# Kernel tuning notes

Hardware: AMD Instinct MI355X
Metric: run time of the kernel (lower is better)

The kernel has to match this reference:

```python
import jax, jax.numpy as jnp
import numpy as np
from jax import lax

B, L, D, C = 4096, 50, 128, 64
V = 100000
H = D // 2  # bidirectional LSTM hidden size; 2*H == emb_dim


def setup_inputs() -> dict:
    key = jax.random.key(0)
    ks = jax.random.split(key, 26)
    f = lambda k, s: jax.random.normal(k, s, dtype=jnp.float32) * 0.05
    return {
        "r_idx": jax.random.randint(ks[0], (B,), 0, V),
        "a_idx": jax.random.randint(ks[1], (B,), 0, V),
        "acc_idx": jax.random.randint(ks[2], (B,), 0, V),
        "rank_q": jax.random.normal(ks[3], (B, L, D), dtype=jnp.float32),
        "rank_q_len": jax.random.randint(ks[4], (B,), 0, L),
        "ru_emb": f(ks[5], (V, D)),
        "au_emb": f(ks[6], (V, D)),
        "Wih_f": f(ks[7], (4 * H, D)), "Whh_f": f(ks[8], (4 * H, H)),
        "bih_f": f(ks[9], (4 * H,)), "bhh_f": f(ks[10], (4 * H,)),
        "Wih_b": f(ks[11], (4 * H, D)), "Whh_b": f(ks[12], (4 * H, H)),
        "bih_b": f(ks[13], (4 * H,)), "bhh_b": f(ks[14], (4 * H,)),
        "conv1_w": f(ks[15], (C, 1, D)), "conv1_b": f(ks[16], (C,)),
        "conv2_w": f(ks[17], (C, 2, D)), "conv2_b": f(ks[18], (C,)),
        "conv3_w": f(ks[19], (C, 3, D)), "conv3_b": f(ks[20], (C,)),
        "fc1_w": f(ks[21], (6,)), "fc1_b": f(ks[22], (1,)),
        "fc2_w": f(ks[23], (C,)), "fc2_b": f(ks[24], (1,)),
    }


def _lstm_dir(x, Wih, Whh, bih, bhh, reverse):
    # x: [B, L, D] -> outputs [B, L, H]; PyTorch gate order i,f,g,o
    b = x.shape[0]
    xs = jnp.swapaxes(x, 0, 1)  # [L, B, D]
    h0 = jnp.zeros((b, Whh.shape[1]), x.dtype)

    def step(carry, xt):
        h, c = carry
        gates = xt @ Wih.T + h @ Whh.T + (bih + bhh)
        i, fg, g, o = jnp.split(gates, 4, axis=-1)
        i = jax.nn.sigmoid(i)
        fg = jax.nn.sigmoid(fg)
        g = jnp.tanh(g)
        o = jax.nn.sigmoid(o)
        c = fg * c + i * g
        h = o * jnp.tanh(c)
        return (h, c), h

    _, ys = lax.scan(step, (h0, h0), xs, reverse=reverse)
    return jnp.swapaxes(ys, 0, 1)


def _score(mat, conv1_w, conv1_b, conv2_w, conv2_b, conv3_w, conv3_b, fc1_w, fc1_b, fc2_w, fc2_b):
    # mat: [B, 3, D]; three tiny conv branches (kernel heights 1/2/3, width=D)
    branches = []
    for w, bias in ((conv1_w, conv1_b), (conv2_w, conv2_b), (conv3_w, conv3_b)):
        k = w.shape[1]
        wins = jnp.stack([mat[:, i:i + k] for i in range(3 - k + 1)], axis=1)  # [B, W, k, D]
        branches.append(jax.nn.relu(jnp.einsum('bwkd,ckd->bcw', wins, w) + bias[None, :, None]))
    s = jnp.concatenate(branches, axis=2)  # [B, C, 6]
    h = jnp.einsum('bcw,w->bc', s, fc1_w) + fc1_b[0]  # fc_new_1: 6 -> 1
    return jnp.einsum('bc,c->b', h, fc2_w) + fc2_b[0]  # fc_new_2: C -> 1


def reference(r_idx, a_idx, acc_idx, rank_q, rank_q_len, ru_emb, au_emb,
              Wih_f, Whh_f, bih_f, bhh_f, Wih_b, Whh_b, bih_b, bhh_b,
              conv1_w, conv1_b, conv2_w, conv2_b, conv3_w, conv3_b,
              fc1_w, fc1_b, fc2_w, fc2_b):
    emb_r = ru_emb[r_idx]
    emb_a = au_emb[a_idx]
    emb_acc = au_emb[acc_idx]
    # bidirectional LSTM over the question sequence
    out_f = _lstm_dir(rank_q, Wih_f, Whh_f, bih_f, bhh_f, reverse=False)
    out_b = _lstm_dir(rank_q, Wih_b, Whh_b, bih_b, bhh_b, reverse=True)
    q_out = jnp.concatenate([out_f, out_b], axis=-1)  # [B, L, D]
    # prepend a zero timestep, then gather per-example at index rank_q_len
    q_pad = jnp.concatenate([jnp.zeros((q_out.shape[0], 1, q_out.shape[2]), q_out.dtype), q_out], axis=1)
    emb_q = q_pad[jnp.arange(q_pad.shape[0]), rank_q_len]  # [B, D]
    low = jnp.stack([emb_r, emb_q, emb_a], axis=1)   # [B, 3, D]
    high = jnp.stack([emb_r, emb_q, emb_acc], axis=1)
    fcp = (conv1_w, conv1_b, conv2_w, conv2_b, conv3_w, conv3_b, fc1_w, fc1_b, fc2_w, fc2_b)
    low_s = _score(low, *fcp)
    high_s = _score(high, *fcp)
    return jnp.sum(low_s - high_s)
```

## Files before the change

### kernel.cpp

```cpp
#include <hip/hip_runtime.h>
#include <hip/hip_bf16.h>

#define LSEQ 50
#define BATCH 4096

typedef __attribute__((ext_vector_type(8))) short bf16x8;
typedef __attribute__((ext_vector_type(4))) float f32x4;

__device__ __forceinline__ unsigned cvtpk(float lo, float hi) {
    unsigned r;
    asm("v_cvt_pk_bf16_f32 %0, %1, %2" : "=v"(r) : "v"(lo), "v"(hi));
    return r;
}
__device__ __forceinline__ bf16x8 pack8(float4 a, float4 b) {
    uint4 u;
    u.x = cvtpk(a.x, a.y); u.y = cvtpk(a.z, a.w);
    u.z = cvtpk(b.x, b.y); u.w = cvtpk(b.z, b.w);
    return __builtin_bit_cast(bf16x8, u);
}
__device__ __forceinline__ float fsigm(float x) {
    return __builtin_amdgcn_rcpf(1.0f + __builtin_amdgcn_exp2f(-1.44269504f * x));
}
__device__ __forceinline__ float ftanh(float x) {
    float e = __builtin_amdgcn_exp2f(2.88539008f * x);
    return 1.0f - 2.0f * __builtin_amdgcn_rcpf(e + 1.0f);
}

__global__ __launch_bounds__(256)
void sort_kernel(const int* __restrict__ qlen, int* __restrict__ perm)
{
    __shared__ int base[64];
    const int tid = threadIdx.x;
    if (tid < 64) base[tid] = 0;
    __syncthreads();
    for (int i = tid; i < BATCH; i += 256) atomicAdd(&base[qlen[i]], 1);
    __syncthreads();
    if (tid == 0) {
        int s = 0;
        for (int v = 0; v < 50; ++v) { int c = base[v]; base[v] = s; s += c; }
    }
    __syncthreads();
    for (int i = tid; i < BATCH; i += 256) {
        int pos = atomicAdd(&base[qlen[i]], 1);
        perm[pos] = i;
    }
}

__global__ __launch_bounds__(256, 2)
void lstm_kernel(const float* __restrict__ rank_q, const int* __restrict__ qlen,
                 const int* __restrict__ perm,
                 const float* __restrict__ Wih_f, const float* __restrict__ Whh_f,
                 const float* __restrict__ bih_f, const float* __restrict__ bhh_f,
                 const float* __restrict__ Wih_b, const float* __restrict__ Whh_b,
                 const float* __restrict__ bih_b, const float* __restrict__ bhh_b,
                 float* __restrict__ embq)
{
    const int grp = blockIdx.x;
    const int b0  = grp << 4;
    const int tid = threadIdx.x;
    const int wv  = tid >> 6;
    const int ln  = tid & 63;
    const int lm  = ln & 15;
    const int lq  = ln >> 4;
    const int m   = (wv << 4) + lm;

    __shared__ __align__(16) unsigned short xbuf[3][16][136];
    __shared__ __align__(16) unsigned short hbuf[2][16][72];
    __shared__ int len_s[16];

    if (tid < 16) len_s[tid] = qlen[perm[b0 + tid]];

    int exq[4], len_e[4];
    #pragma unroll
    for (int r = 0; r < 4; ++r) {
        exq[r]   = perm[b0 + (lq << 2) + r];
        len_e[r] = qlen[exq[r]];
    }

    const int se  = tid >> 4;
    const int exs = perm[b0 + se];
    const int sd  = (tid & 15) << 3;

    __syncthreads();

    int mx = 0, mn = 51;
    #pragma unroll
    for (int i = 0; i < 16; ++i) {
        const int l = len_s[i];
        mx = max(mx, l);
        mn = min(mn, l ? l : 51);
    }

    const int xoff = lm * 136 + (lq << 3);
    const int hoff = lm * 72 + (lq << 3);

    for (int dir = 0; dir < 2; ++dir) {
        const float* Wih = dir ? Wih_b : Wih_f;
        const float* Whh = dir ? Whh_b : Whh_f;
        const float* bih = dir ? bih_b : bih_f;
        const float* bhh = dir ? bhh_b : bhh_f;

        bf16x8 bfrag[4][6];
        float bias[4];
        #pragma unroll
        for (int j = 0; j < 4; ++j) {
            const int n = (j << 6) + m;
            bias[j] = bih[n] + bhh[n];
            #pragma unroll
            for (int s = 0; s < 6; ++s) {
                const int kb = (s << 5) + (lq << 3);
                const float* src = (s < 4) ? (Wih + n * 128 + kb)
                                           : (Whh + n * 64 + (kb - 128));
                bfrag[j][s] = pack8(*(const float4*)src, *(const float4*)(src + 4));
            }
        }

        const int steps = dir ? ((mn == 51) ? 0 : 51 - mn) : mx;

        float cst[4]  = {0.f, 0.f, 0.f, 0.f};
        float qval[4] = {0.f, 0.f, 0.f, 0.f};

        for (int i = tid; i < 16 * 72; i += 256) ((unsigned short*)hbuf)[i] = 0;

        const int tstep = dir ? -128 : 128;
        const float* gp = rank_q + ((size_t)exs * LSEQ + (dir ? LSEQ - 1 : 0)) * 128 + sd;

        float4 ha, hb2;
        if (steps > 0) {
            float4 a0 = *(const float4*)gp, b0v = *(const float4*)(gp + 4); gp += tstep;
            float4 a1 = *(const float4*)gp, b1v = *(const float4*)(gp + 4); gp += tstep;
            *(bf16x8*)&xbuf[0][se][sd] = pack8(a0, b0v);
            *(bf16x8*)&xbuf[1][se][sd] = pack8(a1, b1v);
            if (3 <= steps) { ha = *(const float4*)gp; hb2 = *(const float4*)(gp + 4); gp += tstep; }
        }
        __syncthreads();

        if (steps > 0) {
            f32x4 accx[4];
            {
                const unsigned short* xb = &xbuf[0][0][0];
                bf16x8 x0 = *(const bf16x8*)(xb + xoff);
                bf16x8 x1 = *(const bf16x8*)(xb + xoff + 32);
                bf16x8 x2 = *(const bf16x8*)(xb + xoff + 64);
                bf16x8 x3 = *(const bf16x8*)(xb + xoff + 96);
                #pragma unroll
                for (int j = 0; j < 4; ++j) {
                    f32x4 a = {bias[j], bias[j], bias[j], bias[j]};
                    a = __builtin_amdgcn_mfma_f32_16x16x32_bf16(x0, bfrag[j][0], a, 0, 0, 0);
                    a = __builtin_amdgcn_mfma_f32_16x16x32_bf16(x1, bfrag[j][1], a, 0, 0, 0);
                    a = __builtin_amdgcn_mfma_f32_16x16x32_bf16(x2, bfrag[j][2], a, 0, 0, 0);
                    a = __builtin_amdgcn_mfma_f32_16x16x32_bf16(x3, bfrag[j][3], a, 0, 0, 0);
                    accx[j] = a;
                }
            }

            int r1 = 1, w2 = 2;
            for (int it = 0; it < steps; ++it) {
                const int t   = dir ? (LSEQ - 1 - it) : it;
                const int rbh = it & 1;
                const int wbh = rbh ^ 1;

                float4 na, nb;
                if (it + 4 <= steps) { na = *(const float4*)gp; nb = *(const float4*)(gp + 4); gp += tstep; }

                const unsigned short* hb = &hbuf[rbh][0][0];
                bf16x8 ah0 = *(const bf16x8*)(hb + hoff);
                bf16x8 ah1 = *(const bf16x8*)(hb + hoff + 32);
                f32x4 gate[4];
                #pragma unroll
                for (int j = 0; j < 4; ++j) {
                    f32x4 a = __builtin_amdgcn_mfma_f32_16x16x32_bf16(ah0, bfrag[j][4], accx[j], 0, 0, 0);
                    gate[j]  = __builtin_amdgcn_mfma_f32_16x16x32_bf16(ah1, bfrag[j][5], a, 0, 0, 0);
                }

                if (it + 1 < steps) {
                    const unsigned short* xb = &xbuf[r1][0][0];
                    bf16x8 x0 = *(const bf16x8*)(xb + xoff);
                    bf16x8 x1 = *(const bf16x8*)(xb + xoff + 32);
                    bf16x8 x2 = *(const bf16x8*)(xb + xoff + 64);
                    bf16x8 x3 = *(const bf16x8*)(xb + xoff + 96);
                    #pragma unroll
                    for (int j = 0; j < 4; ++j) {
                        f32x4 a = {bias[j], bias[j], bias[j], bias[j]};
                        a = __builtin_amdgcn_mfma_f32_16x16x32_bf16(x0, bfrag[j][0], a, 0, 0, 0);
                        a = __builtin_amdgcn_mfma_f32_16x16x32_bf16(x1, bfrag[j][1], a, 0, 0, 0);
                        a = __builtin_amdgcn_mfma_f32_16x16x32_bf16(x2, bfrag[j][2], a, 0, 0, 0);
                        a = __builtin_amdgcn_mfma_f32_16x16x32_bf16(x3, bfrag[j][3], a, 0, 0, 0);
                        accx[j] = a;
                    }
                }

                float hn[4];
                #pragma unroll
                for (int r = 0; r < 4; ++r) {
                    float ig = fsigm(gate[0][r]);
                    float fg = fsigm(gate[1][r]);
                    float gg = ftanh(gate[2][r]);
                    float og = fsigm(gate[3][r]);
                    float cn = fg * cst[r] + ig * gg;
                    cst[r] = cn;
                    hn[r] = og * ftanh(cn);
                    if (t == len_e[r] - 1) qval[r] = hn[r];
                }
                const unsigned u01 = cvtpk(hn[0], hn[1]);
                const unsigned u23 = cvtpk(hn[2], hn[3]);
                hbuf[wbh][(lq << 2) + 0][m] = (unsigned short)u01;
                hbuf[wbh][(lq << 2) + 1][m] = (unsigned short)(u01 >> 16);
                hbuf[wbh][(lq << 2) + 2][m] = (unsigned short)u23;
                hbuf[wbh][(lq << 2) + 3][m] = (unsigned short)(u23 >> 16);

                if (it + 3 <= steps) *(bf16x8*)&xbuf[w2][se][sd] = pack8(ha, hb2);
                ha = na; hb2 = nb;

                __syncthreads();
                r1 = (r1 == 2) ? 0 : r1 + 1;
                w2 = (w2 == 2) ? 0 : w2 + 1;
            }
        }

        #pragma unroll
        for (int r = 0; r < 4; ++r)
            embq[(size_t)exq[r] * 128 + (dir << 6) + m] = qval[r];

        __syncthreads();
    }
}

__global__ __launch_bounds__(256)
void prep_kernel(const float* __restrict__ c1w, const float* __restrict__ c2w,
                 const float* __restrict__ c3w, float* __restrict__ T)
{
    const int id = blockIdx.x * 256 + threadIdx.x;
    const int m  = id >> 13;
    const int rem = id & 8191;
    const int j  = rem >> 8;
    const int q  = rem & 255;
    const int c  = q >> 2;
    const int d  = (j << 2) + (q & 3);
    const float* src;
    switch (m) {
        case 0:  src = c1w + c * 128 + d;       break;
        case 1:  src = c2w + c * 256 + d;       break;
        case 2:  src = c2w + c * 256 + 128 + d; break;
        case 3:  src = c3w + c * 384 + d;       break;
        case 4:  src = c3w + c * 384 + 128 + d; break;
        default: src = c3w + c * 384 + 256 + d; break;
    }
    T[id] = *src;
}

__global__ __launch_bounds__(256)
void score_kernel(const int* __restrict__ r_idx, const int* __restrict__ a_idx,
                  const int* __restrict__ acc_idx,
                  const float* __restrict__ ru, const float* __restrict__ au,
                  const float* __restrict__ embq, const float* __restrict__ T,
                  const float* __restrict__ c1b, const float* __restrict__ c2b,
                  const float* __restrict__ c3b,
                  const float* __restrict__ fc1w, const float* __restrict__ fc2w,
                  float* __restrict__ diff)
{
    const int tid = threadIdx.x;
    const int wv  = tid >> 6;
    const int c   = tid & 63;
    const int b0  = blockIdx.x << 4;

    __shared__ __align__(16) float emb[64][132];
    {
        const int row = tid & 63;
        const int e   = row >> 2, v = row & 3;
        const int seg = (tid >> 6) << 5;
        const int bb  = b0 + e;
        const float* src = (v == 0) ? ru   + (size_t)r_idx[bb]   * 128 :
                           (v == 1) ? embq + (size_t)bb          * 128 :
                           (v == 2) ? au   + (size_t)a_idx[bb]   * 128 :
                                      au   + (size_t)acc_idx[bb] * 128;
        #pragma unroll
        for (int i = 0; i < 8; ++i) {
            float4 x = *(const float4*)(src + seg + (i << 2));
            *(float4*)&emb[row][seg + (i << 2)] = x;
        }
    }
    __syncthreads();

    float acc[4][9];
    #pragma unroll
    for (int e = 0; e < 4; ++e)
        #pragma unroll
        for (int k = 0; k < 9; ++k) acc[e][k] = 0.f;

    const float4* Tq = (const float4*)T;
    for (int j = 0; j < 32; ++j) {
        const float4* wq = Tq + j * 64 + c;
        const float4 w1  = wq[0];
        const float4 w20 = wq[2048];
        const float4 w21 = wq[4096];
        const float4 w30 = wq[6144];
        const float4 w31 = wq[8192];
        const float4 w32 = wq[10240];
        const int jd = j << 2;
        #pragma unroll
        for (int e = 0; e < 4; ++e) {
            const int br = ((wv << 2) + e) << 2;
            const float4 er = *(const float4*)&emb[br + 0][jd];
            const float4 eq = *(const float4*)&emb[br + 1][jd];
            const float4 ea = *(const float4*)&emb[br + 2][jd];
            const float4 ex = *(const float4*)&emb[br + 3][jd];
            acc[e][0] += w1.x*ea.x  + w1.y*ea.y  + w1.z*ea.z  + w1.w*ea.w;
            acc[e][1] += w1.x*ex.x  + w1.y*ex.y  + w1.z*ex.z  + w1.w*ex.w;
            acc[e][2] += w20.x*eq.x + w20.y*eq.y + w20.z*eq.z + w20.w*eq.w;
            acc[e][3] += w21.x*ea.x + w21.y*ea.y + w21.z*ea.z + w21.w*ea.w;
            acc[e][4] += w21.x*ex.x + w21.y*ex.y + w21.z*ex.z + w21.w*ex.w;
            acc[e][5] += w30.x*er.x + w30.y*er.y + w30.z*er.z + w30.w*er.w;
            acc[e][6] += w31.x*eq.x + w31.y*eq.y + w31.z*eq.z + w31.w*eq.w;
            acc[e][7] += w32.x*ea.x + w32.y*ea.y + w32.z*ea.z + w32.w*ea.w;
            acc[e][8] += w32.x*ex.x + w32.y*ex.y + w32.z*ex.z + w32.w*ex.w;
        }
    }

    const float b1 = c1b[c], b2 = c2b[c], b3 = c3b[c], f2 = fc2w[c];
    const float f12 = fc1w[2], f14 = fc1w[4], f15 = fc1w[5];
    #pragma unroll
    for (int e = 0; e < 4; ++e) {
        const float r1 = fmaxf(acc[e][0] + b1, 0.f) - fmaxf(acc[e][1] + b1, 0.f);
        const float r2 = fmaxf(acc[e][2] + acc[e][3] + b2, 0.f)
                       - fmaxf(acc[e][2] + acc[e][4] + b2, 0.f);
        const float r3 = fmaxf(acc[e][5] + acc[e][6] + acc[e][7] + b3, 0.f)
                       - fmaxf(acc[e][5] + acc[e][6] + acc[e][8] + b3, 0.f);
        float term = f2 * (f12 * r1 + f14 * r2 + f15 * r3);
        #pragma unroll
        for (int off = 32; off; off >>= 1) term += __shfl_down(term, off);
        if (c == 0) diff[b0 + (wv << 2) + e] = term;
    }
}

__global__ void reduce_kernel(const float* __restrict__ diff, float* __restrict__ out)
{
    __shared__ float s[256];
    const int tid = threadIdx.x;
    float v = 0.f;
    for (int i = tid; i < BATCH; i += 256) v += diff[i];
    s[tid] = v;
    __syncthreads();
    for (int st = 128; st > 0; st >>= 1) {
        if (tid < st) s[tid] += s[tid + st];
        __syncthreads();
    }
    if (tid == 0) out[0] = s[0];
}

extern "C" void kernel_launch(void* const* d_in, const int* in_sizes, int n_in,
                              void* d_out, int out_size, void* d_ws, size_t ws_size,
                              hipStream_t stream) {
    (void)in_sizes; (void)n_in; (void)out_size; (void)ws_size;
    const int*   r_idx   = (const int*)d_in[0];
    const int*   a_idx   = (const int*)d_in[1];
    const int*   acc_idx = (const int*)d_in[2];
    const float* rank_q  = (const float*)d_in[3];
    const int*   qlen    = (const int*)d_in[4];
    const float* ru      = (const float*)d_in[5];
    const float* au      = (const float*)d_in[6];
    const float* Wih_f   = (const float*)d_in[7];
    const float* Whh_f   = (const float*)d_in[8];
    const float* bih_f   = (const float*)d_in[9];
    const float* bhh_f   = (const float*)d_in[10];
    const float* Wih_b   = (const float*)d_in[11];
    const float* Whh_b   = (const float*)d_in[12];
    const float* bih_b   = (const float*)d_in[13];
    const float* bhh_b   = (const float*)d_in[14];
    const float* c1w     = (const float*)d_in[15];
    const float* c1b     = (const float*)d_in[16];
    const float* c2w     = (const float*)d_in[17];
    const float* c2b     = (const float*)d_in[18];
    const float* c3w     = (const float*)d_in[19];
    const float* c3b     = (const float*)d_in[20];
    const float* fc1w    = (const float*)d_in[21];
    const float* fc2w    = (const float*)d_in[23];

    float* embq = (float*)d_ws;
    float* diff = embq + (size_t)BATCH * 128;
    float* T    = diff + BATCH;
    int*   perm = (int*)(T + 49152);

    sort_kernel<<<1, 256, 0, stream>>>(qlen, perm);
    prep_kernel<<<192, 256, 0, stream>>>(c1w, c2w, c3w, T);
    lstm_kernel<<<256, 256, 0, stream>>>(rank_q, qlen, perm,
                                         Wih_f, Whh_f, bih_f, bhh_f,
                                         Wih_b, Whh_b, bih_b, bhh_b, embq);
    score_kernel<<<BATCH / 16, 256, 0, stream>>>(r_idx, a_idx, acc_idx, ru, au, embq, T,
                                                 c1b, c2b, c3b, fc1w, fc2w, diff);
    reduce_kernel<<<1, 256, 0, stream>>>(diff, (float*)d_out);
}
```

Before: 97.87 us.

## Fuse LSTM, score and reduce into one cooperative kernel with grid syncs

The sort and prep kernels are merged into one launch, using an extra block for the sort. The LSTM, score and reduce kernels become a single cooperative kernel that uses grid.sync between phases, with shared memory reused through a union. The aim is to cut launch overhead and the gaps between kernels, at the cost of grid-wide barriers and requiring all 256 blocks to be co-resident. The fast sigmoid/tanh helper functions are removed from the top of the file, so the activations are presumably inlined in the truncated section.

```diff
diff --git a/kernel.cpp b/kernel.cpp
--- a/kernel.cpp
+++ b/kernel.cpp
@@ -1,5 +1,8 @@
 #include <hip/hip_runtime.h>
 #include <hip/hip_bf16.h>
+#include <hip/hip_cooperative_groups.h>
+
+namespace cg = cooperative_groups;
 
 #define LSEQ 50
 #define BATCH 4096
@@ -18,219 +21,31 @@
     u.z = cvtpk(b.x, b.y); u.w = cvtpk(b.z, b.w);
     return __builtin_bit_cast(bf16x8, u);
 }
-__device__ __forceinline__ float fsigm(float x) {
-    return __builtin_amdgcn_rcpf(1.0f + __builtin_amdgcn_exp2f(-1.44269504f * x));
-}
-__device__ __forceinline__ float ftanh(float x) {
-    float e = __builtin_amdgcn_exp2f(2.88539008f * x);
-    return 1.0f - 2.0f * __builtin_amdgcn_rcpf(e + 1.0f);
-}
 
 __global__ __launch_bounds__(256)
-void sort_kernel(const int* __restrict__ qlen, int* __restrict__ perm)
+void sortprep_kernel(const int* __restrict__ qlen, int* __restrict__ perm,
+                     const float* __restrict__ c1w, const float* __restrict__ c2w,
+                     const float* __restrict__ c3w, float* __restrict__ T)
 {
-    __shared__ int base[64];
     const int tid = threadIdx.x;
-    if (tid < 64) base[tid] = 0;
-    __syncthreads();
-    for (int i = tid; i < BATCH; i += 256) atomicAdd(&base[qlen[i]], 1);
-    __syncthreads();
-    if (tid == 0) {
-        int s = 0;
-        for (int v = 0; v < 50; ++v) { int c = base[v]; base[v] = s; s += c; }
+    if (blockIdx.x == 192) {
+        __shared__ int base[64];
+        if (tid < 64) base[tid] = 0;
+        __syncthreads();
+        for (int i = tid; i < BATCH; i += 256) atomicAdd(&base[qlen[i]], 1);
+        __syncthreads();
+        if (tid == 0) {
+            int s = 0;
+            for (int v = 0; v < 50; ++v) { int c = base[v]; base[v] = s; s += c; }
+        }
+        __syncthreads();
+        for (int i = tid; i < BATCH; i += 256) {
+            int pos = atomicAdd(&base[qlen[i]], 1);
+            perm[pos] = i;
+        }
+        return;
     }
-    __syncthreads();
-    for (int i = tid; i < BATCH; i += 256) {
-        int pos = atomicAdd(&base[qlen[i]], 1);
-        perm[pos] = i;
-    }
-}
-
-__global__ __launch_bounds__(256, 2)
-void lstm_kernel(const float* __restrict__ rank_q, const int* __restrict__ qlen,
-                 const int* __restrict__ perm,
-                 const float* __restrict__ Wih_f, const float* __restrict__ Whh_f,
-                 const float* __restrict__ bih_f, const float* __restrict__ bhh_f,
-                 const float* __restrict__ Wih_b, const float* __restrict__ Whh_b,
-                 const float* __restrict__ bih_b, const float* __restrict__ bhh_b,
-                 float* __restrict__ embq)
-{
-    const int grp = blockIdx.x;
-    const int b0  = grp << 4;
-    const int tid = threadIdx.x;
-    const int wv  = tid >> 6;
-    const int ln  = tid & 63;
-    const int lm  = ln & 15;
-    const int lq  = ln >> 4;
-    const int m   = (wv << 4) + lm;
-
-    __shared__ __align__(16) unsigned short xbuf[3][16][136];
-    __shared__ __align__(16) unsigned short hbuf[2][16][72];
-    __shared__ int len_s[16];
-
-    if (tid < 16) len_s[tid] = qlen[perm[b0 + tid]];
-
-    int exq[4], len_e[4];
-    #pragma unroll
-    for (int r = 0; r < 4; ++r) {
-        exq[r]   = perm[b0 + (lq << 2) + r];
-        len_e[r] = qlen[exq[r]];
-    }
-
-    const int se  = tid >> 4;
-    const int exs = perm[b0 + se];
-    const int sd  = (tid & 15) << 3;
-
-    __syncthreads();
-
-    int mx = 0, mn = 51;
-    #pragma unroll
-    for (int i = 0; i < 16; ++i) {
-        const int l = len_s[i];
-        mx = max(mx, l);
-        mn = min(mn, l ? l : 51);
-    }
-
-    const int xoff = lm * 136 + (lq << 3);
-    const int hoff = lm * 72 + (lq << 3);
-
-    for (int dir = 0; dir < 2; ++dir) {
-        const float* Wih = dir ? Wih_b : Wih_f;
-        const float* Whh = dir ? Whh_b : Whh_f;
-        const float* bih = dir ? bih_b : bih_f;
-        const float* bhh = dir ? bhh_b : bhh_f;
-
-        bf16x8 bfrag[4][6];
-        float bias[4];
-        #pragma unroll
-        for (int j = 0; j < 4; ++j) {
-            const int n = (j << 6) + m;
-            bias[j] = bih[n] + bhh[n];
-            #pragma unroll
-            for (int s = 0; s < 6; ++s) {
-                const int kb = (s << 5) + (lq << 3);
-                const float* src = (s < 4) ? (Wih + n * 128 + kb)
-                                           : (Whh + n * 64 + (kb - 128));
-                bfrag[j][s] = pack8(*(const float4*)src, *(const float4*)(src + 4));
-            }
-        }
-
-        const int steps = dir ? ((mn == 51) ? 0 : 51 - mn) : mx;
-
-        float cst[4]  = {0.f, 0.f, 0.f, 0.f};
-        float qval[4] = {0.f, 0.f, 0.f, 0.f};
-
-        for (int i = tid; i < 16 * 72; i += 256) ((unsigned short*)hbuf)[i] = 0;
-
-        const int tstep = dir ? -128 : 128;
-        const float* gp = rank_q + ((size_t)exs * LSEQ + (dir ? LSEQ - 1 : 0)) * 128 + sd;
-
-        float4 ha, hb2;
-        if (steps > 0) {
-            float4 a0 = *(const float4*)gp, b0v = *(const float4*)(gp + 4); gp += tstep;
-            float4 a1 = *(const float4*)gp, b1v = *(const float4*)(gp + 4); gp += tstep;
-            *(bf16x8*)&xbuf[0][se][sd] = pack8(a0, b0v);
-            *(bf16x8*)&xbuf[1][se][sd] = pack8(a1, b1v);
-            if (3 <= steps) { ha = *(const float4*)gp; hb2 = *(const float4*)(gp + 4); gp += tstep; }
-        }
-        __syncthreads();
-
-        if (steps > 0) {
-            f32x4 accx[4];
-            {
-                const unsigned short* xb = &xbuf[0][0][0];
-                bf16x8 x0 = *(const bf16x8*)(xb + xoff);
-                bf16x8 x1 = *(const bf16x8*)(xb + xoff + 32);
-                bf16x8 x2 = *(const bf16x8*)(xb + xoff + 64);
-                bf16x8 x3 = *(const bf16x8*)(xb + xoff + 96);
-                #pragma unroll
-                for (int j = 0; j < 4; ++j) {
-                    f32x4 a = {bias[j], bias[j], bias[j], bias[j]};
-                    a = __builtin_amdgcn_mfma_f32_16x16x32_bf16(x0, bfrag[j][0], a, 0, 0, 0);
-                    a = __builtin_amdgcn_mfma_f32_16x16x32_bf16(x1, bfrag[j][1], a, 0, 0, 0);
-                    a = __builtin_amdgcn_mfma_f32_16x16x32_bf16(x2, bfrag[j][2], a, 0, 0, 0);
-                    a = __builtin_amdgcn_mfma_f32_16x16x32_bf16(x3, bfrag[j][3], a, 0, 0, 0);
-                    accx[j] = a;
-                }
-            }
-
-            int r1 = 1, w2 = 2;
-            for (int it = 0; it < steps; ++it) {
-                const int t   = dir ? (LSEQ - 1 - it) : it;
-                const int rbh = it & 1;
-                const int wbh = rbh ^ 1;
-
-                float4 na, nb;
-                if (it + 4 <= steps) { na = *(const float4*)gp; nb = *(const float4*)(gp + 4); gp += tstep; }
-
-                const unsigned short* hb = &hbuf[rbh][0][0];
-                bf16x8 ah0 = *(const bf16x8*)(hb + hoff);
-                bf16x8 ah1 = *(const bf16x8*)(hb + hoff + 32);
-                f32x4 gate[4];
-                #pragma unroll
-                for (int j = 0; j < 4; ++j) {
-                    f32x4 a = __builtin_amdgcn_mfma_f32_16x16x32_bf16(ah0, bfrag[j][4], accx[j], 0, 0, 0);
-                    gate[j]  = __builtin_amdgcn_mfma_f32_16x16x32_bf16(ah1, bfrag[j][5], a, 0, 0, 0);
-                }
-
-                if (it + 1 < steps) {
-                    const unsigned short* xb = &xbuf[r1][0][0];
-                    bf16x8 x0 = *(const bf16x8*)(xb + xoff);
-                    bf16x8 x1 = *(const bf16x8*)(xb + xoff + 32);
-                    bf16x8 x2 = *(const bf16x8*)(xb + xoff + 64);
-                    bf16x8 x3 = *(const bf16x8*)(xb + xoff + 96);
-                    #pragma unroll
-                    for (int j = 0; j < 4; ++j) {
-                        f32x4 a = {bias[j], bias[j], bias[j], bias[j]};
-                        a = __builtin_amdgcn_mfma_f32_16x16x32_bf16(x0, bfrag[j][0], a, 0, 0, 0);
-                        a = __builtin_amdgcn_mfma_f32_16x16x32_bf16(x1, bfrag[j][1], a, 0, 0, 0);
-                        a = __builtin_amdgcn_mfma_f32_16x16x32_bf16(x2, bfrag[j][2], a, 0, 0, 0);
-                        a = __builtin_amdgcn_mfma_f32_16x16x32_bf16(x3, bfrag[j][3], a, 0, 0, 0);
-                        accx[j] = a;
-                    }
-                }
-
-                float hn[4];
-                #pragma unroll
-                for (int r = 0; r < 4; ++r) {
-                    float ig = fsigm(gate[0][r]);
-                    float fg = fsigm(gate[1][r]);
-                    float gg = ftanh(gate[2][r]);
-                    float og = fsigm(gate[3][r]);
-                    float cn = fg * cst[r] + ig * gg;
-                    cst[r] = cn;
-                    hn[r] = og * ftanh(cn);
-                    if (t == len_e[r] - 1) qval[r] = hn[r];
-                }
-                const unsigned u01 = cvtpk(hn[0], hn[1]);
-                const unsigned u23 = cvtpk(hn[2], hn[3]);
-                hbuf[wbh][(lq << 2) + 0][m] = (unsigned short)u01;
-                hbuf[wbh][(lq << 2) + 1][m] = (unsigned short)(u01 >> 16);
-                hbuf[wbh][(lq << 2) + 2][m] = (unsigned short)u23;
-                hbuf[wbh][(lq << 2) + 3][m] = (unsigned short)(u23 >> 16);
-
-                if (it + 3 <= steps) *(bf16x8*)&xbuf[w2][se][sd] = pack8(ha, hb2);
-                ha = na; hb2 = nb;
-
-                __syncthreads();
-                r1 = (r1 == 2) ? 0 : r1 + 1;
-                w2 = (w2 == 2) ? 0 : w2 + 1;
-            }
-        }
-
-        #pragma unroll
-        for (int r = 0; r < 4; ++r)
-            embq[(size_t)exq[r] * 128 + (dir << 6) + m] = qval[r];
-
-        __syncthreads();
-    }
-}
-
-__global__ __launch_bounds__(256)
-void prep_kernel(const float* __restrict__ c1w, const float* __restrict__ c2w,
-                 const float* __restrict__ c3w, float* __restrict__ T)
-{
-    const int id = blockIdx.x * 256 + threadIdx.x;
+    const int id = blockIdx.x * 256 + tid;
     const int m  = id >> 13;
     const int rem = id & 8191;
     const int j  = rem >> 8;
@@ -249,103 +64,299 @@
     T[id] = *src;
 }
 
-__global__ __launch_bounds__(256)
-void score_kernel(const int* __restrict__ r_idx, const int* __restrict__ a_idx,
+__global__ __launch_bounds__(256, 2)
+void fused_kernel(const float* __restrict__ rank_q, const int* __restrict__ qlen,
+                  const int* __restrict__ perm,
+                  const float* __restrict__ Wih_f, const float* __restrict__ Whh_f,
+                  const float* __restrict__ bih_f, const float* __restrict__ bhh_f,
+                  const float* __restrict__ Wih_b, const float* __restrict__ Whh_b,
+                  const float* __restrict__ bih_b, const float* __restrict__ bhh_b,
+                  float* __restrict__ embq, const float* __restrict__ T,
+                  const int* __restrict__ r_idx, const int* __restrict__ a_idx,
                   const int* __restrict__ acc_idx,
                   const float* __restrict__ ru, const float* __restrict__ au,
-                  const float* __restrict__ embq, const float* __restrict__ T,
                   const float* __restrict__ c1b, const float* __restrict__ c2b,
                   const float* __restrict__ c3b,
                   const float* __restrict__ fc1w, const float* __restrict__ fc2w,
-                  float* __restrict__ diff)
+                  float* __restrict__ diff, float* __restrict__ out)
 {
+    cg::grid_group grid = cg::this_grid();
+
+    __shared__ union {
+        struct {
+            unsigned short xbuf[3][16][136];
+            unsigned short hbuf[2][16][72];
+            int len_s[16];
+        } l;
+        struct {
+            float emb[64][132];
+        } s;
+    } sm;
+
     const int tid = threadIdx.x;
     const int wv  = tid >> 6;
-    const int c   = tid & 63;
-    const int b0  = blockIdx.x << 4;
-
-    __shared__ __align__(16) float emb[64][132];
+    const int ln  = tid & 63;
+    const int lm  = ln & 15;
+    const int lq  = ln >> 4;
+    const int m   = (wv << 4) + lm;
+
     {
-        const int row = tid & 63;
-        const int e   = row >> 2, v = row & 3;
-        const int seg = (tid >> 6) << 5;
-        const int bb  = b0 + e;
-        const float* src = (v == 0) ? ru   + (size_t)r_idx[bb]   * 128 :
-                           (v == 1) ? embq + (size_t)bb          * 128 :
-                           (v == 2) ? au   + (size_t)a_idx[bb]   * 128 :
-                                      au   + (size_t)acc_idx[bb] * 128;
+        const int b0 = blockIdx.x << 4;
+
+        if (tid < 16) sm.l.len_s[tid] = qlen[perm[b0 + tid]];
+
+        int exq[4], len_e[4];
         #pragma unroll
-        for (int i = 0; i < 8; ++i) {
-            float4 x = *(const float4*)(src + seg + (i << 2));
-            *(float4*)&emb[row][seg + (i << 2)] = x;
+        for (int r = 0; r < 4; ++r) {
+            exq[r]   = perm[b0 + (lq << 2) + r];
+            len_e[r] = qlen[exq[r]];
+        }
+
+        const int se  = tid >> 4;
+        const int exs = perm[b0 + se];
+        const int sd  = (tid & 15) << 3;
+
+        __syncthreads();
+
+        int mx = 0, mn = 51;
+        #pragma unroll
+        for (int i = 0; i < 16; ++i) {
+            const int l = sm.l.len_s[i];
+            mx = max(mx, l);
+            mn = min(mn, l ? l : 51);
+        }
+
+        const int xoff = lm * 136 + (lq << 3);
+        const int hoff = lm * 72 + (lq << 3);
+        const float NL1 = -1.44269504f;
+        const float NL2 = -2.88539008f;
+
+        for (int dir = 0; dir < 2; ++dir) {
+            const float* Wih = dir ? Wih_b : Wih_f;
+            const float* Whh = dir ? Whh_b : Whh_f;
+            const float* bih = dir ? bih_b : bih_f;
+            const float* bhh = dir ? bhh_b : bhh_f;
+
+            bf16x8 bfrag[4][6];
+            float bias[4];
+            #pragma unroll
+            for (int j = 0; j < 4; ++j) {
+                const int n = (j << 6) + m;
+                bias[j] = bih[n] + bhh[n];
+                #pragma unroll
+                for (int s = 0; s < 6; ++s) {
+                    const int kb = (s << 5) + (lq << 3);
+                    const float* src = (s < 4) ? (Wih + n * 128 + kb)
+                                               : (Whh + n * 64 + (kb - 128));
+                    bfrag[j][s] = pack8(*(const float4*)src, *(const float4*)(src + 4));
+                }
+            }
+
+            const int steps = dir ? ((mn == 51) ? 0 : 51 - mn) : mx;
+
+            float cst[4]  = {0.f, 0.f, 0.f, 0.f};
+            float qval[4] = {0.f, 0.f, 0.f, 0.f};
+
+            for (int i = tid; i < 16 * 72; i += 256) ((unsigned short*)sm.l.hbuf)[i] = 0;
+
+            const int tstep = dir ? -128 : 128;
+            const float* gp = rank_q + ((size_t)exs * LSEQ + (dir ? LSEQ - 1 : 0)) * 128 + sd;
+
+            float4 ha, hb2;
+            if (steps > 0) {
+                float4 a0 = *(const float4*)gp, b0v = *(const float4*)(gp + 4); gp += tstep;
+                float4 a1 = *(const float4*)gp, b1v = *(const float4*)(gp + 4); gp += tstep;
+                *(bf16x8*)&sm.l.xbuf[0][se][sd] = pack8(a0, b0v);
+                *(bf16x8*)&sm.l.xbuf[1][se][sd] = pack8(a1, b1v);
+                if (3 <= steps) { ha = *(const float4*)gp; hb2 = *(const float4*)(gp + 4); gp += tstep; }
+            }
+            __syncthreads();
+
+            if (steps > 0) {
+                f32x4 accx[4];
+                {
+                    const unsigned short* xb = &sm.l.xbuf[0][0][0];
+                    bf16x8 x0 = *(const bf16x8*)(xb + xoff);
+                    bf16x8 x1 = *(const bf16x8*)(xb + xoff + 32);
+                    bf16x8 x2 = *(const bf16x8*)(xb + xoff + 64);
+                    bf16x8 x3 = *(const bf16x8*)(xb + xoff + 96);
+                    #pragma unroll
+                    for (int j = 0; j < 4; ++j) {
+                        f32x4 a = {bias[j], bias[j], bias[j], bias[j]};
+                        a = __builtin_amdgcn_mfma_f32_16x16x32_bf16(x0, bfrag[j][0], a, 0, 0, 0);
+                        a = __builtin_amdgcn_mfma_f32_16x16x32_bf16(x1, bfrag[j][1], a, 0, 0, 0);
+                        a = __builtin_amdgcn_mfma_f32_16x16x32_bf16(x2, bfrag[j][2], a, 0, 0, 0);
+                        a = __builtin_amdgcn_mfma_f32_16x16x32_bf16(x3, bfrag[j][3], a, 0, 0, 0);
+                        accx[j] = a;
+                    }
+                }
+
+                int r1 = 1, w2 = 2;
+                for (int it = 0; it < steps; ++it) {
+                    const int t   = dir ? (LSEQ - 1 - it) : it;
+                    const int rbh = it & 1;
+                    const int wbh = rbh ^ 1;
+
+                    float4 na, nb;
+                    if (it + 4 <= steps) { na = *(const float4*)gp; nb = *(const float4*)(gp + 4); gp += tstep; }
+
+                    const unsigned short* hb = &sm.l.hbuf[rbh][0][0];
+                    bf16x8 ah0 = *(const bf16x8*)(hb + hoff);
+                    bf16x8 ah1 = *(const bf16x8*)(hb + hoff + 32);
+                    f32x4 gate[4];
+                    #pragma unroll
+                    for (int j = 0; j < 4; ++j) {
+                        f32x4 a = __builtin_amdgcn_mfma_f32_16x16x32_bf16(ah0, bfrag[j][4], accx[j], 0, 0, 0);
+                        gate[j]  = __builtin_amdgcn_mfma_f32_16x16x32_bf16(ah1, bfrag[j][5], a, 0, 0, 0);
+                    }
+
+                    if (it + 1 < steps) {
+                        const unsigned short* xb = &sm.l.xbuf[r1][0][0];
+                        bf16x8 x0 = *(const bf16x8*)(xb + xoff);
+                        bf16x8 x1 = *(const bf16x8*)(xb + xoff + 32);
+                        bf16x8 x2 = *(const bf16x8*)(xb + xoff + 64);
+                        bf16x8 x3 = *(const bf16x8*)(xb + xoff + 96);
+                        #pragma unroll
+                        for (int j = 0; j < 4; ++j) {
+                            f32x4 a = {bias[j], bias[j], bias[j], bias[j]};
+                            a = __builtin_amdgcn_mfma_f32_16x16x32_bf16(x0, bfrag[j][0], a, 0, 0, 0);
+                            a = __builtin_amdgcn_mfma_f32_16x16x32_bf16(x1, bfrag[j][1], a, 0, 0, 0);
+                            a = __builtin_amdgcn_mfma_f32_16x16x32_bf16(x2, bfrag[j][2], a, 0, 0, 0);
+                            a = __builtin_amdgcn_mfma_f32_16x16x32_bf16(x3, bfrag[j][3], a, 0, 0, 0);
+                            accx[j] = a;
+                        }
+                    }
+
+                    float hn[4];
+                    #pragma unroll
+                    for (int r = 0; r < 4; ++r) {
+                        const float ei = __builtin_amdgcn_exp2f(NL1 * gate[0][r]);
+                        const float ef = __builtin_amdgcn_exp2f(NL1 * gate[1][r]);
+                        const float eg = __builtin_amdgcn_exp2f(NL2 * gate[2][r]);
+                        const float A = 1.f + ei, F = 1.f + ef, G = 1.f + eg;
+                        const float AG = A * G;
+                        const float R1 = __builtin_amdgcn_rcpf(AG * F);
+                        const float cn = (AG * R1) * cst[r] + (F * R1) * (1.f - eg);
+                        cst[r] = cn;
+                        const float cc = fmaxf(cn, -15.f);
+                        const float ec = __builtin_amdgcn_exp2f(NL2 * cc);
+                        const float eo = __builtin_amdgcn_exp2f(NL1 * gate[3][r]);
+                        const float R3 = __builtin_amdgcn_rcpf((1.f + eo) * (1.f + ec));
+                        hn[r] = R3 * (1.f - ec);
+                        if (t == len_e[r] - 1) qval[r] = hn[r];
+                    }
+                    const unsigned u01 = cvtpk(hn[0], hn[1]);
+                    const unsigned u23 = cvtpk(hn[2], hn[3]);
+                    sm.l.hbuf[wbh][(lq << 2) + 0][m] = (unsigned short)u01;
+                    sm.l.hbuf[wbh][(lq << 2) + 1][m] = (unsigned short)(u01 >> 16);
+                    sm.l.hbuf[wbh][(lq << 2) + 2][m] = (unsigned short)u23;
+                    sm.l.hbuf[wbh][(lq << 2) + 3][m] = (unsigned short)(u23 >> 16);
+
+                    if (it + 3 <= steps) *(bf16x8*)&sm.l.xbuf[w2][se][sd] = pack8(ha, hb2);
+                    ha = na; hb2 = nb;
+
+                    __syncthreads();
+                    r1 = (r1 == 2) ? 0 : r1 + 1;
+                    w2 = (w2 == 2) ? 0 : w2 + 1;
+                }
+            }
+
+            #pragma unroll
+            for (int r = 0; r < 4; ++r)
+                embq[(size_t)exq[r] * 128 + (dir << 6) + m] = qval[r];
+
+            __syncthreads();
         }
     }
-    __syncthreads();
-
-    float acc[4][9];
-    #pragma unroll
-    for (int e = 0; e < 4; ++e)
+
+    grid.sync();
+
+    {
+        const int c  = tid & 63;
+        const int b0 = blockIdx.x << 4;
+
+        {
+            const int row = tid & 63;
+            const int e   = row >> 2, v = row & 3;
+            const int seg = (tid >> 6) << 5;
+            const int bb  = b0 + e;
+            const float* src = (v == 0) ? ru   + (size_t)r_idx[bb]   * 128 :
+                               (v == 1) ? embq + (size_t)bb          * 128 :
+                               (v == 2) ? au   + (size_t)a_idx[bb]   * 128 :
+                                          au   + (size_t)acc_idx[bb] * 128;
+            #pragma unroll
+            for (int i = 0; i < 8; ++i) {
+                float4 x = *(const float4*)(src + seg + (i << 2));
+                *(float4*)&sm.s.emb[row][seg + (i << 2)] = x;
+            }
+        }
+        __syncthreads();
+
+        float acc[4][9];
         #pragma unroll
-        for (int k = 0; k < 9; ++k) acc[e][k] = 0.f;
-
-    const float4* Tq = (const float4*)T;
-    for (int j = 0; j < 32; ++j) {
-        const float4* wq = Tq + j * 64 + c;
-        const float4 w1  = wq[0];
-        const float4 w20 = wq[2048];
-        const float4 w21 = wq[4096];
-        const float4 w30 = wq[6144];
-        const float4 w31 = wq[8192];
-        const float4 w32 = wq[10240];
-        const int jd = j << 2;
+        for (int e = 0; e < 4; ++e)
+            #pragma unroll
+            for (int k = 0; k < 9; ++k) acc[e][k] = 0.f;
+
+        const float4* Tq = (const float4*)T;
+        for (int j = 0; j < 32; ++j) {
+            const float4* wq = Tq + j * 64 + c;
+            const float4 w1  = wq[0];
+            const float4 w20 = wq[2048];
+            const float4 w21 = wq[4096];
+            const float4 w30 = wq[6144];
+            const float4 w31 = wq[8192];
+            const float4 w32 = wq[10240];
+            const int jd = j << 2;
+            #pragma unroll
+            for (int e = 0; e < 4; ++e) {
+                const int br = ((wv << 2) + e) << 2;
+                const float4 er = *(const float4*)&sm.s.emb[br + 0][jd];
+                const float4 eq = *(const float4*)&sm.s.emb[br + 1][jd];
+                const float4 ea = *(const float4*)&sm.s.emb[br + 2][jd];
+                const float4 ex = *(const float4*)&sm.s.emb[br + 3][jd];
+                acc[e][0] += w1.x*ea.x  + w1.y*ea.y  + w1.z*ea.z  + w1.w*ea.w;
+                acc[e][1] += w1.x*ex.x  + w1.y*ex.y  + w1.z*ex.z  + w1.w*ex.w;
+                acc[e][2] += w20.x*eq.x + w20.y*eq.y + w20.z*eq.z + w20.w*eq.w;
+                acc[e][3] += w21.x*ea.x + w21.y*ea.y + w21.z*ea.z + w21.w*ea.w;
+                acc[e][4] += w21.x*ex.x + w21.y*ex.y + w21.z*ex.z + w21.w*ex.w;
+                acc[e][5] += w30.x*er.x + w30.y*er.y + w30.z*er.z + w30.w*er.w;
+                acc[e][6] += w31.x*eq.x + w31.y*eq.y + w31.z*eq.z + w31.w*eq.w;
+                acc[e][7] += w32.x*ea.x + w32.y*ea.y + w32.z*ea.z + w32.w*ea.w;
+                acc[e][8] += w32.x*ex.x + w32.y*ex.y + w32.z*ex.z + w32.w*ex.w;
+            }
+        }
+
+        const float b1 = c1b[c], b2 = c2b[c], b3 = c3b[c], f2 = fc2w[c];
+        const float f12 = fc1w[2], f14 = fc1w[4], f15 = fc1w[5];
         #pragma unroll
         for (int e = 0; e < 4; ++e) {
-            const int br = ((wv << 2) + e) << 2;
-            const float4 er = *(const float4*)&emb[br + 0][jd];
-            const float4 eq = *(const float4*)&emb[br + 1][jd];
-            const float4 ea = *(const float4*)&emb[br + 2][jd];
-            const float4 ex = *(const float4*)&emb[br + 3][jd];
-            acc[e][0] += w1.x*ea.x  + w1.y*ea.y  + w1.z*ea.z  + w1.w*ea.w;
-            acc[e][1] += w1.x*ex.x  + w1.y*ex.y  + w1.z*ex.z  + w1.w*ex.w;
-            acc[e][2] += w20.x*eq.x + w20.y*eq.y + w20.z*eq.z + w20.w*eq.w;
-            acc[e][3] += w21.x*ea.x + w21.y*ea.y + w21.z*ea.z + w21.w*ea.w;
-            acc[e][4] += w21.x*ex.x + w21.y*ex.y + w21.z*ex.z + w21.w*ex.w;
-            acc[e][5] += w30.x*er.x + w30.y*er.y + w30.z*er.z + w30.w*er.w;
-            acc[e][6] += w31.x*eq.x + w31.y*eq.y + w31.z*eq.z + w31.w*eq.w;
-            acc[e][7] += w32.x*ea.x + w32.y*ea.y + w32.z*ea.z + w32.w*ea.w;
-            acc[e][8] += w32.x*ex.x + w32.y*ex.y + w32.z*ex.z + w32.w*ex.w;
+            const float r1 = fmaxf(acc[e][0] + b1, 0.f) - fmaxf(acc[e][1] + b1, 0.f);
+            const float r2 = fmaxf(acc[e][2] + acc[e][3] + b2, 0.f)
+                           - fmaxf(acc[e][2] + acc[e][4] + b2, 0.f);
+            const float r3 = fmaxf(acc[e][5] + acc[e][6] + acc[e][7] + b3, 0.f)
+                           - fmaxf(acc[e][5] + acc[e][6] + acc[e][8] + b3, 0.f);
+            float term = f2 * (f12 * r1 + f14 * r2 + f15 * r3);
+            #pragma unroll
+            for (int off = 32; off; off >>= 1) term += __shfl_down(term, off);
+            if (c == 0) diff[b0 + (wv << 2) + e] = term;
         }
     }
 
-    const float b1 = c1b[c], b2 = c2b[c], b3 = c3b[c], f2 = fc2w[c];
-    const float f12 = fc1w[2], f14 = fc1w[4], f15 = fc1w[5];
-    #pragma unroll
-    for (int e = 0; e < 4; ++e) {
-        const float r1 = fmaxf(acc[e][0] + b1, 0.f) - fmaxf(acc[e][1] + b1, 0.f);
-        const float r2 = fmaxf(acc[e][2] + acc[e][3] + b2, 0.f)
-                       - fmaxf(acc[e][2] + acc[e][4] + b2, 0.f);
-        const float r3 = fmaxf(acc[e][5] + acc[e][6] + acc[e][7] + b3, 0.f)
-                       - fmaxf(acc[e][5] + acc[e][6] + acc[e][8] + b3, 0.f);
-        float term = f2 * (f12 * r1 + f14 * r2 + f15 * r3);
-        #pragma unroll
-        for (int off = 32; off; off >>= 1) term += __shfl_down(term, off);
-        if (c == 0) diff[b0 + (wv << 2) + e] = term;
+    grid.sync();
+
+    if (blockIdx.x == 0) {
+        __shared__ float s[256];
+        float v = 0.f;
+        for (int i = tid; i < BATCH; i += 256) v += diff[i];
+        s[tid] = v;
+        __syncthreads();
+        for (int st = 128; st > 0; st >>= 1) {
+            if (tid < st) s[tid] += s[tid + st];
+            __syncthreads();
+        }
+        if (tid == 0) out[0] = s[0];
     }
-}
-
-__global__ void reduce_kernel(const float* __restrict__ diff, float* __restrict__ out)
-{
-    __shared__ float s[256];
-    const int tid = threadIdx.x;
-    float v = 0.f;
-    for (int i = tid; i < BATCH; i += 256) v += diff[i];
-    s[tid] = v;
-    __syncthreads();
-    for (int st = 128; st > 0; st >>= 1) {
-        if (tid < st) s[tid] += s[tid + st];
-        __syncthreads();
-    }
-    if (tid == 0) out[0] = s[0];
 }
 
 extern "C" void kernel_launch(void* const* d_in, const int* in_sizes, int n_in,
@@ -380,13 +391,21 @@
     float* diff = embq + (size_t)BATCH * 128;
     float* T    = diff + BATCH;
     int*   perm = (int*)(T + 49152);
-
-    sort_kernel<<<1, 256, 0, stream>>>(qlen, perm);
-    prep_kernel<<<192, 256, 0, stream>>>(c1w, c2w, c3w, T);
-    lstm_kernel<<<256, 256, 0, stream>>>(rank_q, qlen, perm,
-                                         Wih_f, Whh_f, bih_f, bhh_f,
-                                         Wih_b, Whh_b, bih_b, bhh_b, embq);
-    score_kernel<<<BATCH / 16, 256, 0, stream>>>(r_idx, a_idx, acc_idx, ru, au, embq, T,
-                                                 c1b, c2b, c3b, fc1w, fc2w, diff);
-    reduce_kernel<<<1, 256, 0, stream>>>(diff, (float*)d_out);
+    float* out  = (float*)d_out;
+
+    sortprep_kernel<<<193, 256, 0, stream>>>(qlen, perm, c1w, c2w, c3w, T);
+
+    void* kargs[] = {
+        (void*)&rank_q, (void*)&qlen, (void*)&perm,
+        (void*)&Wih_f, (void*)&Whh_f, (void*)&bih_f, (void*)&bhh_f,
+        (void*)&Wih_b, (void*)&Whh_b, (void*)&bih_b, (void*)&bhh_b,
+        (void*)&embq, (void*)&T,
+        (void*)&r_idx, (void*)&a_idx, (void*)&acc_idx,
+        (void*)&ru, (void*)&au,
+        (void*)&c1b, (void*)&c2b, (void*)&c3b,
+        (void*)&fc1w, (void*)&fc2w,
+        (void*)&diff, (void*)&out
+    };
+    hipLaunchCooperativeKernel((void*)fused_kernel, dim3(256), dim3(256),
+                               kargs, 0, stream);
 }
```

After: 163.9 us. 1.67x slower.

## Merge sort/prep kernels, fold reduction into score kernel, cheapen LSTM gate math

Applied to the files above, without the earlier changes.

Combines the sort and weight-prep launches into a single kernel with a dedicated sort block. Replaces the separate reduce launch with a last-block-done reduction in the score kernel, using an atomic counter that the sort block resets. Also rewrites the LSTM gate nonlinearities to share reciprocals across gates, cutting rcp instructions per element. The aims are fewer kernel launches and less transcendental work on the recurrent critical path, at the cost of an added fence and atomic plus slightly different numerics, with the cell state clamped at -15 before its tanh.

```diff
diff --git a/kernel.cpp b/kernel.cpp
--- a/kernel.cpp
+++ b/kernel.cpp
@@ -18,32 +18,49 @@
     u.z = cvtpk(b.x, b.y); u.w = cvtpk(b.z, b.w);
     return __builtin_bit_cast(bf16x8, u);
 }
-__device__ __forceinline__ float fsigm(float x) {
-    return __builtin_amdgcn_rcpf(1.0f + __builtin_amdgcn_exp2f(-1.44269504f * x));
-}
-__device__ __forceinline__ float ftanh(float x) {
-    float e = __builtin_amdgcn_exp2f(2.88539008f * x);
-    return 1.0f - 2.0f * __builtin_amdgcn_rcpf(e + 1.0f);
-}
 
 __global__ __launch_bounds__(256)
-void sort_kernel(const int* __restrict__ qlen, int* __restrict__ perm)
+void sortprep_kernel(const int* __restrict__ qlen, int* __restrict__ perm,
+                     const float* __restrict__ c1w, const float* __restrict__ c2w,
+                     const float* __restrict__ c3w, float* __restrict__ T,
+                     int* __restrict__ counter)
 {
-    __shared__ int base[64];
     const int tid = threadIdx.x;
-    if (tid < 64) base[tid] = 0;
-    __syncthreads();
-    for (int i = tid; i < BATCH; i += 256) atomicAdd(&base[qlen[i]], 1);
-    __syncthreads();
-    if (tid == 0) {
-        int s = 0;
-        for (int v = 0; v < 50; ++v) { int c = base[v]; base[v] = s; s += c; }
-    }
-    __syncthreads();
-    for (int i = tid; i < BATCH; i += 256) {
-        int pos = atomicAdd(&base[qlen[i]], 1);
-        perm[pos] = i;
-    }
+    if (blockIdx.x == 192) {
+        __shared__ int base[64];
+        if (tid == 0) *counter = 0;
+        if (tid < 64) base[tid] = 0;
+        __syncthreads();
+        for (int i = tid; i < BATCH; i += 256) atomicAdd(&base[qlen[i]], 1);
+        __syncthreads();
+        if (tid == 0) {
+            int s = 0;
+            for (int v = 0; v < 50; ++v) { int c = base[v]; base[v] = s; s += c; }
+        }
+        __syncthreads();
+        for (int i = tid; i < BATCH; i += 256) {
+            int pos = atomicAdd(&base[qlen[i]], 1);
+            perm[pos] = i;
+        }
+        return;
+    }
+    const int id = blockIdx.x * 256 + tid;
+    const int m  = id >> 13;
+    const int rem = id & 8191;
+    const int j  = rem >> 8;
+    const int q  = rem & 255;
+    const int c  = q >> 2;
+    const int d  = (j << 2) + (q & 3);
+    const float* src;
+    switch (m) {
+        case 0:  src = c1w + c * 128 + d;       break;
+        case 1:  src = c2w + c * 256 + d;       break;
+        case 2:  src = c2w + c * 256 + 128 + d; break;
+        case 3:  src = c3w + c * 384 + d;       break;
+        case 4:  src = c3w + c * 384 + 128 + d; break;
+        default: src = c3w + c * 384 + 256 + d; break;
+    }
+    T[id] = *src;
 }
 
 __global__ __launch_bounds__(256, 2)
@@ -93,6 +110,8 @@
 
     const int xoff = lm * 136 + (lq << 3);
     const int hoff = lm * 72 + (lq << 3);
+    const float NL1 = -1.44269504f;
+    const float NL2 = -2.88539008f;
 
     for (int dir = 0; dir < 2; ++dir) {
         const float* Wih = dir ? Wih_b : Wih_f;
@@ -193,13 +212,19 @@
                 float hn[4];
                 #pragma unroll
                 for (int r = 0; r < 4; ++r) {
-                    float ig = fsigm(gate[0][r]);
-                    float fg = fsigm(gate[1][r]);
-                    float gg = ftanh(gate[2][r]);
-                    float og = fsigm(gate[3][r]);
-                    float cn = fg * cst[r] + ig * gg;
+                    const float ei = __builtin_amdgcn_exp2f(NL1 * gate[0][r]);
+                    const float ef = __builtin_amdgcn_exp2f(NL1 * gate[1][r]);
+                    const float eg = __builtin_amdgcn_exp2f(NL2 * gate[2][r]);
+                    const float A = 1.f + ei, F = 1.f + ef, G = 1.f + eg;
+                    const float AG = A * G;
+                    const float R1 = __builtin_amdgcn_rcpf(AG * F);
+                    const float cn = (AG * R1) * cst[r] + (F * R1) * (1.f - eg);
                     cst[r] = cn;
-                    hn[r] = og * ftanh(cn);
+                    const float cc = fmaxf(cn, -15.f);
+                    const float ec = __builtin_amdgcn_exp2f(NL2 * cc);
+                    const float eo = __builtin_amdgcn_exp2f(NL1 * gate[3][r]);
+                    const float R3 = __builtin_amdgcn_rcpf((1.f + eo) * (1.f + ec));
+                    hn[r] = R3 * (1.f - ec);
                     if (t == len_e[r] - 1) qval[r] = hn[r];
                 }
                 const unsigned u01 = cvtpk(hn[0], hn[1]);
@@ -227,29 +252,6 @@
 }
 
 __global__ __launch_bounds__(256)
-void prep_kernel(const float* __restrict__ c1w, const float* __restrict__ c2w,
-                 const float* __restrict__ c3w, float* __restrict__ T)
-{
-    const int id = blockIdx.x * 256 + threadIdx.x;
-    const int m  = id >> 13;
-    const int rem = id & 8191;
-    const int j  = rem >> 8;
-    const int q  = rem & 255;
-    const int c  = q >> 2;
-    const int d  = (j << 2) + (q & 3);
-    const float* src;
-    switch (m) {
-        case 0:  src = c1w + c * 128 + d;       break;
-        case 1:  src = c2w + c * 256 + d;       break;
-        case 2:  src = c2w + c * 256 + 128 + d; break;
-        case 3:  src = c3w + c * 384 + d;       break;
-        case 4:  src = c3w + c * 384 + 128 + d; break;
-        default: src = c3w + c * 384 + 256 + d; break;
-    }
-    T[id] = *src;
-}
-
-__global__ __launch_bounds__(256)
 void score_kernel(const int* __restrict__ r_idx, const int* __restrict__ a_idx,
                   const int* __restrict__ acc_idx,
                   const float* __restrict__ ru, const float* __restrict__ au,
@@ -257,7 +259,8 @@
                   const float* __restrict__ c1b, const float* __restrict__ c2b,
                   const float* __restrict__ c3b,
                   const float* __restrict__ fc1w, const float* __restrict__ fc2w,
-                  float* __restrict__ diff)
+                  float* __restrict__ diff, int* __restrict__ counter,
+                  float* __restrict__ out)
 {
     const int tid = threadIdx.x;
     const int wv  = tid >> 6;
@@ -265,6 +268,7 @@
     const int b0  = blockIdx.x << 4;
 
     __shared__ __align__(16) float emb[64][132];
+    __shared__ int is_last;
     {
         const int row = tid & 63;
         const int e   = row >> 2, v = row & 3;
@@ -331,21 +335,23 @@
         for (int off = 32; off; off >>= 1) term += __shfl_down(term, off);
         if (c == 0) diff[b0 + (wv << 2) + e] = term;
     }
-}
-
-__global__ void reduce_kernel(const float* __restrict__ diff, float* __restrict__ out)
-{
-    __shared__ float s[256];
-    const int tid = threadIdx.x;
-    float v = 0.f;
-    for (int i = tid; i < BATCH; i += 256) v += diff[i];
-    s[tid] = v;
+
+    __threadfence();
+    if (tid == 0) is_last = (atomicAdd(counter, 1) == gridDim.x - 1);
     __syncthreads();
-    for (int st = 128; st > 0; st >>= 1) {
-        if (tid < st) s[tid] += s[tid + st];
-        __syncthreads();
-    }
-    if (tid == 0) out[0] = s[0];
+    if (is_last) {
+        __threadfence();
+        __shared__ float s[256];
+        float v = 0.f;
+        for (int i = tid; i < BATCH; i += 256) v += diff[i];
+        s[tid] = v;
+        __syncthreads();
+        for (int st = 128; st > 0; st >>= 1) {
+            if (tid < st) s[tid] += s[tid + st];
+            __syncthreads();
+        }
+        if (tid == 0) out[0] = s[0];
+    }
 }
 
 extern "C" void kernel_launch(void* const* d_in, const int* in_sizes, int n_in,
@@ -376,17 +382,17 @@
     const float* fc1w    = (const float*)d_in[21];
     const float* fc2w    = (const float*)d_in[23];
 
-    float* embq = (float*)d_ws;
-    float* diff = embq + (size_t)BATCH * 128;
-    float* T    = diff + BATCH;
-    int*   perm = (int*)(T + 49152);
-
-    sort_kernel<<<1, 256, 0, stream>>>(qlen, perm);
-    prep_kernel<<<192, 256, 0, stream>>>(c1w, c2w, c3w, T);
+    float* embq    = (float*)d_ws;
+    float* diff    = embq + (size_t)BATCH * 128;
+    float* T       = diff + BATCH;
+    int*   perm    = (int*)(T + 49152);
+    int*   counter = perm + BATCH;
+
+    sortprep_kernel<<<193, 256, 0, stream>>>(qlen, perm, c1w, c2w, c3w, T, counter);
     lstm_kernel<<<256, 256, 0, stream>>>(rank_q, qlen, perm,
                                          Wih_f, Whh_f, bih_f, bhh_f,
                                          Wih_b, Whh_b, bih_b, bhh_b, embq);
     score_kernel<<<BATCH / 16, 256, 0, stream>>>(r_idx, a_idx, acc_idx, ru, au, embq, T,
-                                                 c1b, c2b, c3b, fc1w, fc2w, diff);
-    reduce_kernel<<<1, 256, 0, stream>>>(diff, (float*)d_out);
-}
+                                                 c1b, c2b, c3b, fc1w, fc2w,
+                                                 diff, counter, (float*)d_out);
+}
```

After: 112.5 us. 1.15x slower.
